# Performance work log

Measured on AMD Instinct MI355X. Metric: run time of the kernel, lower is better.

Reference implementation:

```python
import jax, jax.numpy as jnp
import numpy as np
from jax import lax

V = 50000          # vocab
E = 64             # embedding_dim
B = 64             # batch
SEQ = 1024         # sentence length
NC = 6             # num_classes
L = 4              # num_layers (total conv layers)
KTOP = 4
NF = [10, 14, 18, 22]          # num_filters per stage
KS = [7, 5, 5, 3]              # kernel sizes
ROWS = [E // 2**i for i in range(5)]   # [64,32,16,8,4]
GROUPS = ROWS[:4]              # conv_i groups = rows[i-1]
# dynamic k-max schedule: k_l = max(k_top, ceil((L-l)/L * SEQ)) for l=1,2,3; last pool uses k_top
KPOOL = [max(KTOP, int(np.ceil((L - l) / L * SEQ))) for l in (1, 2, 3)] + [KTOP]  # [768,512,256,4]


def _uniform(key, shape, fan):
    s = 1.0 / np.sqrt(fan)
    return jax.random.uniform(key, shape, jnp.float32, -s, s)


def setup_inputs() -> dict:
    key = jax.random.key(0)
    ks = jax.random.split(key, 16)
    tokens = jax.random.randint(ks[0], (B, SEQ), 0, V)
    emb = jax.random.normal(ks[1], (V, E), jnp.float32)
    inp = {"tokens": tokens, "emb": emb}
    # conv weights: OIH layout, I = in_channels / groups = num_filters[i-1] (or 1 for conv1)
    in_pg = [1, NF[0], NF[1], NF[2]]
    out_ch = [NF[i] * ROWS[i] for i in range(4)]   # [640,448,288,176]
    for i in range(4):
        fan = in_pg[i] * KS[i]
        inp[f"w{i+1}"] = _uniform(ks[2 + 2 * i], (out_ch[i], in_pg[i], KS[i]), fan)
        inp[f"b{i+1}"] = _uniform(ks[3 + 2 * i], (out_ch[i],), fan)
    fc_in = ROWS[4] * NF[3] * KTOP   # 4*22*4 = 352
    inp["fcw"] = _uniform(ks[10], (NC, fc_in), fc_in)
    inp["fcb"] = _uniform(ks[11], (NC,), fc_in)
    return inp


def _fold(x, nf):
    # channel index c = row*nf + filt; sum adjacent rows pairwise (Fold(2,2))
    b, d, s = x.shape
    r = d // nf
    return x.reshape(b, r // 2, 2, nf, s).sum(axis=2).reshape(b, d // 2, s)


def _kmax(x, k):
    # top-k along seq axis, preserving original temporal order
    _, idx = lax.top_k(x, k)
    idx = jnp.sort(idx, axis=-1)
    return jnp.take_along_axis(x, idx, axis=-1)


def reference(tokens, emb, w1, b1, w2, b2, w3, b3, w4, b4, fcw, fcb):
    x = emb[tokens]                 # (B, S, E)
    x = x.transpose(0, 2, 1)        # (B, E, S)
    ws, bs = (w1, w2, w3, w4), (b1, b2, b3, b4)
    for i in range(4):
        pad = KS[i] - 1             # 'wide' convolution
        x = lax.conv_general_dilated(
            x, ws[i], (1,), [(pad, pad)],
            dimension_numbers=("NCH", "OIH", "NCH"),
            feature_group_count=GROUPS[i],
        ) + bs[i][None, :, None]
        x = _fold(x, NF[i])
        x = _kmax(x, KPOOL[i])
        x = jnp.tanh(x)
    # dropout is identity in eval mode
    x = x.reshape(x.shape[0], -1)   # (B, 352)
    return x @ fcw.T + fcb
```

## Files before the change

kernel.cpp:

```cpp
#include <hip/hip_runtime.h>
#include <hip/hip_bf16.h>
#include <math.h>


#if defined(__has_builtin)
#if __has_builtin(__builtin_amdgcn_ballot_w64)
#define BALLOT64(expr) __builtin_amdgcn_ballot_w64(expr)
#endif
#endif
#ifndef BALLOT64
#define BALLOT64(expr) __ballot(expr)
#endif

__device__ __forceinline__ unsigned f2ord(float f) {
    unsigned u = __float_as_uint(f);
    return (u & 0x80000000u) ? ~u : (u | 0x80000000u);
}
__device__ __forceinline__ float ord2f(unsigned key) {
    unsigned u = (key & 0x80000000u) ? (key & 0x7fffffffu) : ~key;
    return __uint_as_float(u);
}
__device__ __forceinline__ float tanh_fast(float x) {
    float e = __expf(2.f * x);
    return 1.f - 2.f * __builtin_amdgcn_rcpf(e + 1.f);
}
__device__ __forceinline__ int mbcnt64(unsigned long long m) {
    return __builtin_amdgcn_mbcnt_hi((unsigned)(m >> 32),
           __builtin_amdgcn_mbcnt_lo((unsigned)m, 0u));
}

template<int CH>
__device__ __forceinline__ void select_finish(const unsigned* keys, unsigned T,
                                              int k, float* __restrict__ out)
{
    int g = 0, e = 0;
    #pragma unroll
    for (int i = 0; i < CH; ++i) { g += (keys[i] > T); e += (keys[i] == T); }

    int gtBefore = 0, eqBefore = 0, totG = 0;
    #pragma unroll
    for (int b = 0; b < 5; ++b) {
        unsigned long long mg = BALLOT64((((g >> b) & 1) != 0));
        unsigned long long me = BALLOT64((((e >> b) & 1) != 0));
        gtBefore += mbcnt64(mg) << b;
        eqBefore += mbcnt64(me) << b;
        totG     += __popcll(mg) << b;
    }
    const int needTies = k - totG;

    int gRun = 0, eRun = 0;
    #pragma unroll
    for (int i = 0; i < CH; ++i) {
        const unsigned key = keys[i];
        const bool isG = key > T;
        const bool isE = key == T;
        const int eIdx = eqBefore + eRun;
        const int dst = gtBefore + gRun + min(eIdx, needTies);
        if (isG || (isE && eIdx < needTies))
            out[dst] = tanh_fast(ord2f(key));
        gRun += isG; eRun += isE;
    }
}

template<int CH>
__device__ void wave_select2(const unsigned* k0, const unsigned* k1, int k,
                             float* __restrict__ out0, float* __restrict__ out1)
{
    unsigned p0 = 0, p1 = 0;
    #pragma unroll 1
    for (int pos = 31; pos >= 0; --pos) {
        const unsigned bit = 1u << pos;
        const unsigned t0 = p0 | bit, t1 = p1 | bit;
        int c0 = 0, c1 = 0;
        #pragma unroll
        for (int i = 0; i < CH; ++i) {
            c0 += __popcll(BALLOT64((k0[i] >= t0)));
            c1 += __popcll(BALLOT64((k1[i] >= t1)));
        }
        if (c0 >= k) p0 = t0;
        if (c1 >= k) p1 = t1;
    }
    select_finish<CH>(k0, p0, k, out0);
    select_finish<CH>(k1, p1, k, out1);
}

__global__ __launch_bounds__(320, 2) void layer1_fused(
    const int* __restrict__ tokens, const float* __restrict__ emb,
    const float* __restrict__ W1, const float* __restrict__ B1,
    float* __restrict__ Z1)
{
    const int j = blockIdx.x;
    const int b = blockIdx.y;
    const int t = threadIdx.x;
    const int w = t >> 6;
    const int lane = t & 63;

    __shared__ float xr[2][1036];

    const float2* emb2 = (const float2*)emb;
    for (int i = t; i < 1036; i += 320) {
        int s = i - 6;
        float a = 0.f, c = 0.f;
        if (s >= 0 && s < 1024) {
            int tok = tokens[b * 1024 + s];
            float2 v = emb2[(size_t)tok * 32 + j];
            a = v.x; c = v.y;
        }
        xr[0][i] = a;
        xr[1][i] = c;
    }
    __syncthreads();

    const int beg = lane * 17;
    const int len = max(0, min(17, 1030 - beg));

    float x0[23], x1[23];
    #pragma unroll
    for (int i = 0; i < 23; ++i)
        if (i < len + 6) { x0[i] = xr[0][beg + i]; x1[i] = xr[1][beg + i]; }

    unsigned keys0[17], keys1[17];
    #pragma unroll 2
    for (int half = 0; half < 2; ++half) {
        const int f = w + 5 * half;
        float wa[7], wb[7];
        #pragma unroll
        for (int k2 = 0; k2 < 7; ++k2) {
            wa[k2] = W1[(2 * j * 10 + f) * 7 + k2];
            wb[k2] = W1[((2 * j + 1) * 10 + f) * 7 + k2];
        }
        const float bias = B1[2 * j * 10 + f] + B1[(2 * j + 1) * 10 + f];
        unsigned* keys = half ? keys1 : keys0;
        #pragma unroll
        for (int i = 0; i < 17; ++i) {
            if (i < len) {
                float acc = bias;
                #pragma unroll
                for (int k2 = 0; k2 < 7; ++k2)
                    acc += x0[i + k2] * wa[k2] + x1[i + k2] * wb[k2];
                keys[i] = f2ord(acc);
            } else {
                keys[i] = 0u;
            }
        }
    }
    const size_t orow = (size_t)b * 320 + (size_t)j * 10;
    wave_select2<17>(keys0, keys1, 768,
                     Z1 + (orow + w) * 768,
                     Z1 + (orow + w + 5) * 768);
}

template <int IPG, int NF, int K, int SIN, int SOUT, int KSEL, int NW, int CH>
__global__ __launch_bounds__(NW * 64, 2) void conv_fold_select_kernel(
    const float* __restrict__ X, const float* __restrict__ W,
    const float* __restrict__ Bias, float* __restrict__ Z,
    int Cin, int Cfold)
{
    static_assert(NF == 2 * NW, "2 filters per wave");
    static_assert(64 * CH >= SOUT, "chunk covers row");
    constexpr int W2 = 64 * CH + K - 1;

    const int t = threadIdx.x;
    const int j = blockIdx.x;
    const int b = blockIdx.y;
    const int wav = t >> 6, lane = t & 63;

    __shared__ float xs[2 * IPG][W2];

    const float* Xb = X + ((size_t)b * Cin + (size_t)(2 * j) * IPG) * SIN;
    for (int idx = t; idx < 2 * IPG * W2; idx += NW * 64) {
        int r = idx / W2, p = idx - r * W2;
        int sg = p - (K - 1);
        xs[r][p] = (sg >= 0 && sg < SIN) ? Xb[(size_t)r * SIN + sg] : 0.f;
    }
    __syncthreads();

    const int f0 = __builtin_amdgcn_readfirstlane(2 * wav);
    float acc0[CH], acc1[CH];
    {
        float bias0 = Bias[2 * j * NF + f0]     + Bias[(2 * j + 1) * NF + f0];
        float bias1 = Bias[2 * j * NF + f0 + 1] + Bias[(2 * j + 1) * NF + f0 + 1];
        #pragma unroll
        for (int i = 0; i < CH; ++i) { acc0[i] = bias0; acc1[i] = bias1; }
    }
    const int base = lane * CH;

    #pragma unroll 2
    for (int h = 0; h < 2; ++h) {
        const float* Wh = W + (size_t)((2 * j + h) * NF) * IPG * K;
        #pragma unroll 1
        for (int c = 0; c < IPG; ++c) {
            float win[CH + K - 1];
            #pragma unroll
            for (int p = 0; p < CH + K - 1; ++p)
                win[p] = xs[h * IPG + c][base + p];
            #pragma unroll
            for (int k2 = 0; k2 < K; ++k2) {
                const float w0 = Wh[((size_t)f0 * IPG + c) * K + k2];
                const float w1 = Wh[((size_t)(f0 + 1) * IPG + c) * K + k2];
                #pragma unroll
                for (int i = 0; i < CH; ++i) {
                    acc0[i] = fmaf(win[i + k2], w0, acc0[i]);
                    acc1[i] = fmaf(win[i + k2], w1, acc1[i]);
                }
            }
        }
    }

    unsigned keys0[CH], keys1[CH];
    #pragma unroll
    for (int i = 0; i < CH; ++i) {
        keys0[i] = (base + i < SOUT) ? f2ord(acc0[i]) : 0u;
        keys1[i] = (base + i < SOUT) ? f2ord(acc1[i]) : 0u;
    }
    const size_t orow = (size_t)b * Cfold + (size_t)j * NF;
    wave_select2<CH>(keys0, keys1, KSEL,
                     Z + (orow + f0) * (size_t)KSEL,
                     Z + (orow + f0 + 1) * (size_t)KSEL);
}

__global__ __launch_bounds__(192) void fc_kernel(
    const float* __restrict__ Z, const float* __restrict__ Wf,
    const float* __restrict__ bf, float* __restrict__ out)
{
    int g = blockIdx.x * blockDim.x + threadIdx.x;
    if (g >= 64 * 6) return;
    int b = g / 6, c = g % 6;
    float acc = bf[c];
    const float* zr = Z + b * 352;
    const float* wr = Wf + c * 352;
    for (int i = 0; i < 352; ++i) acc += zr[i] * wr[i];
    out[g] = acc;
}

extern "C" void kernel_launch(void* const* d_in, const int* in_sizes, int n_in,
                              void* d_out, int out_size, void* d_ws, size_t ws_size,
                              hipStream_t stream)
{
    const int*   tokens = (const int*)  d_in[0];
    const float* emb    = (const float*)d_in[1];
    const float* w1     = (const float*)d_in[2];
    const float* b1     = (const float*)d_in[3];
    const float* w2     = (const float*)d_in[4];
    const float* b2     = (const float*)d_in[5];
    const float* w3     = (const float*)d_in[6];
    const float* b3     = (const float*)d_in[7];
    const float* w4     = (const float*)d_in[8];
    const float* b4     = (const float*)d_in[9];
    const float* fcw    = (const float*)d_in[10];
    const float* fcb    = (const float*)d_in[11];
    float* out = (float*)d_out;
    float* ws  = (float*)d_ws;

    float* Z1 = ws;
    float* Z2 = ws + 15728640;
    float* Z3 = ws;
    float* Z4 = ws + 2359296;

    layer1_fused<<<dim3(32, 64), 320, 0, stream>>>(tokens, emb, w1, b1, Z1);

    conv_fold_select_kernel<10, 14, 5, 768, 772, 512, 7, 13>
        <<<dim3(16, 64), 7 * 64, 0, stream>>>(Z1, w2, b2, Z2, 320, 224);

    conv_fold_select_kernel<14, 18, 5, 512, 516, 256, 9, 9>
        <<<dim3(8, 64), 9 * 64, 0, stream>>>(Z2, w3, b3, Z3, 224, 144);

    conv_fold_select_kernel<18, 22, 3, 256, 258, 4, 11, 5>
        <<<dim3(4, 64), 11 * 64, 0, stream>>>(Z3, w4, b4, Z4, 144, 88);

    fc_kernel<<<2, 192, 0, stream>>>(Z4, fcw, fcb, out);
}
```

Measured before the change: 380.4 us.

## Add early-exit radix select over N rows; layer1 uses 2 waves x 5 filters

Generalizes the wave-level bitwise radix select to handle N rows at once. It tracks the count above the threshold and the bucket size, so a row stops its bit passes once the bucket exactly equals the remaining k. Layer 1 now runs 2 waves per block, each computing 5 filters, instead of 5 waves with 2 filters each. Its inputs are read straight from shared memory instead of register windows, and launch-bound occupancy hints are dropped. Early exit cuts the 32 ballot passes in the common case, but holding 5 filters of keys per wave raises register pressure and leaves fewer waves per block.

```diff
diff --git a/kernel.cpp b/kernel.cpp
--- a/kernel.cpp
+++ b/kernel.cpp
@@ -62,29 +62,42 @@
     }
 }
 
-template<int CH>
-__device__ void wave_select2(const unsigned* k0, const unsigned* k1, int k,
-                             float* __restrict__ out0, float* __restrict__ out1)
-{
-    unsigned p0 = 0, p1 = 0;
+template<int N, int CH>
+__device__ void wave_selectN(const unsigned (*keys)[CH], int k,
+                             float* const* outs)
+{
+    unsigned p[N];
+    int above[N], buck[N];
+    #pragma unroll
+    for (int n = 0; n < N; ++n) { p[n] = 0u; above[n] = 0; buck[n] = 64 * CH; }
+
+    unsigned doneMask = 0;
+    const unsigned allDone = (1u << N) - 1u;
     #pragma unroll 1
     for (int pos = 31; pos >= 0; --pos) {
-        const unsigned bit = 1u << pos;
-        const unsigned t0 = p0 | bit, t1 = p1 | bit;
-        int c0 = 0, c1 = 0;
-        #pragma unroll
-        for (int i = 0; i < CH; ++i) {
-            c0 += __popcll(BALLOT64((k0[i] >= t0)));
-            c1 += __popcll(BALLOT64((k1[i] >= t1)));
-        }
-        if (c0 >= k) p0 = t0;
-        if (c1 >= k) p1 = t1;
-    }
-    select_finish<CH>(k0, p0, k, out0);
-    select_finish<CH>(k1, p1, k, out1);
-}
-
-__global__ __launch_bounds__(320, 2) void layer1_fused(
+        #pragma unroll
+        for (int n = 0; n < N; ++n) {
+            if (!((doneMask >> n) & 1u)) {
+                const unsigned t = p[n] | (1u << pos);
+                int c = 0;
+                #pragma unroll
+                for (int i = 0; i < CH; ++i)
+                    c += __popcll(BALLOT64((keys[n][i] >= t)));
+                const int inb = c - above[n];
+                const int rem = k - above[n];
+                if (inb >= rem) { p[n] = t; buck[n] = inb; }
+                else            { above[n] += inb; buck[n] -= inb; }
+                if (buck[n] == k - above[n]) doneMask |= (1u << n);
+            }
+        }
+        if (doneMask == allDone) break;
+    }
+    #pragma unroll
+    for (int n = 0; n < N; ++n)
+        select_finish<CH>(keys[n], p[n], k, outs[n]);
+}
+
+__global__ __launch_bounds__(128) void layer1_fused(
     const int* __restrict__ tokens, const float* __restrict__ emb,
     const float* __restrict__ W1, const float* __restrict__ B1,
     float* __restrict__ Z1)
@@ -95,10 +108,10 @@
     const int w = t >> 6;
     const int lane = t & 63;
 
-    __shared__ float xr[2][1036];
+    __shared__ float xr[2][1100];
 
     const float2* emb2 = (const float2*)emb;
-    for (int i = t; i < 1036; i += 320) {
+    for (int i = t; i < 1100; i += 128) {
         int s = i - 6;
         float a = 0.f, c = 0.f;
         if (s >= 0 && s < 1024) {
@@ -112,17 +125,14 @@
     __syncthreads();
 
     const int beg = lane * 17;
-    const int len = max(0, min(17, 1030 - beg));
-
-    float x0[23], x1[23];
-    #pragma unroll
-    for (int i = 0; i < 23; ++i)
-        if (i < len + 6) { x0[i] = xr[0][beg + i]; x1[i] = xr[1][beg + i]; }
-
-    unsigned keys0[17], keys1[17];
-    #pragma unroll 2
-    for (int half = 0; half < 2; ++half) {
-        const int f = w + 5 * half;
+
+    unsigned keys[5][17];
+    float* outs[5];
+    const size_t orow = (size_t)b * 320 + (size_t)j * 10;
+
+    #pragma unroll
+    for (int q = 0; q < 5; ++q) {
+        const int f = 5 * w + q;
         float wa[7], wb[7];
         #pragma unroll
         for (int k2 = 0; k2 < 7; ++k2) {
@@ -130,28 +140,22 @@
             wb[k2] = W1[((2 * j + 1) * 10 + f) * 7 + k2];
         }
         const float bias = B1[2 * j * 10 + f] + B1[(2 * j + 1) * 10 + f];
-        unsigned* keys = half ? keys1 : keys0;
         #pragma unroll
         for (int i = 0; i < 17; ++i) {
-            if (i < len) {
-                float acc = bias;
-                #pragma unroll
-                for (int k2 = 0; k2 < 7; ++k2)
-                    acc += x0[i + k2] * wa[k2] + x1[i + k2] * wb[k2];
-                keys[i] = f2ord(acc);
-            } else {
-                keys[i] = 0u;
-            }
-        }
-    }
-    const size_t orow = (size_t)b * 320 + (size_t)j * 10;
-    wave_select2<17>(keys0, keys1, 768,
-                     Z1 + (orow + w) * 768,
-                     Z1 + (orow + w + 5) * 768);
+            float acc = bias;
+            #pragma unroll
+            for (int k2 = 0; k2 < 7; ++k2)
+                acc += xr[0][beg + i + k2] * wa[k2]
+                     + xr[1][beg + i + k2] * wb[k2];
+            keys[q][i] = (beg + i < 1030) ? f2ord(acc) : 0u;
+        }
+        outs[q] = Z1 + (orow + f) * 768;
+    }
+    wave_selectN<5, 17>(keys, 768, outs);
 }
 
 template <int IPG, int NF, int K, int SIN, int SOUT, int KSEL, int NW, int CH>
-__global__ __launch_bounds__(NW * 64, 2) void conv_fold_select_kernel(
+__global__ __launch_bounds__(NW * 64) void conv_fold_select_kernel(
     const float* __restrict__ X, const float* __restrict__ W,
     const float* __restrict__ Bias, float* __restrict__ Z,
     int Cin, int Cfold)
@@ -207,16 +211,16 @@
         }
     }
 
-    unsigned keys0[CH], keys1[CH];
+    unsigned keys[2][CH];
     #pragma unroll
     for (int i = 0; i < CH; ++i) {
-        keys0[i] = (base + i < SOUT) ? f2ord(acc0[i]) : 0u;
-        keys1[i] = (base + i < SOUT) ? f2ord(acc1[i]) : 0u;
+        keys[0][i] = (base + i < SOUT) ? f2ord(acc0[i]) : 0u;
+        keys[1][i] = (base + i < SOUT) ? f2ord(acc1[i]) : 0u;
     }
     const size_t orow = (size_t)b * Cfold + (size_t)j * NF;
-    wave_select2<CH>(keys0, keys1, KSEL,
-                     Z + (orow + f0) * (size_t)KSEL,
-                     Z + (orow + f0 + 1) * (size_t)KSEL);
+    float* outs[2] = { Z + (orow + f0) * (size_t)KSEL,
+                       Z + (orow + f0 + 1) * (size_t)KSEL };
+    wave_selectN<2, CH>(keys, KSEL, outs);
 }
 
 __global__ __launch_bounds__(192) void fc_kernel(
@@ -257,7 +261,7 @@
     float* Z3 = ws;
     float* Z4 = ws + 2359296;
 
-    layer1_fused<<<dim3(32, 64), 320, 0, stream>>>(tokens, emb, w1, b1, Z1);
+    layer1_fused<<<dim3(32, 64), 128, 0, stream>>>(tokens, emb, w1, b1, Z1);
 
     conv_fold_select_kernel<10, 14, 5, 768, 772, 512, 7, 13>
         <<<dim3(16, 64), 7 * 64, 0, stream>>>(Z1, w2, b2, Z2, 320, 224);
```

Measured after the change: 370.5 us. 2.6% less time.
